# Performance work log

Hardware: AMD Instinct MI355X
Metric: run time of the kernel (lower is better)

## Reference

```python
import jax, jax.numpy as jnp
import numpy as np

VOL = (256, 256, 256)
K = 64  # number of connected components (clusters)


def setup_inputs() -> dict:
    key = jax.random.key(0)
    k1, k2, k3 = jax.random.split(key, 3)
    # Precomputed connected-component labels of (pred + target) > 0.
    # 0 = background, 1..K = clusters.
    labels = jax.random.randint(k1, VOL, 0, K + 1, dtype=jnp.int32)
    fg = labels > 0
    # Binary prediction / ground-truth masks, nonzero only inside labeled regions
    # (consistent with labels being components of the overlay of pred and target).
    pred = ((jax.random.uniform(k2, VOL) < 0.6) & fg).astype(jnp.float32)
    target = ((jax.random.uniform(k3, VOL) < 0.6) & fg).astype(jnp.float32)
    return {"pred": pred, "target": target, "labels": labels, "num_clusters": K}


def reference(pred, target, labels, num_clusters):
    # Per-cluster dice via one fused segment reduction instead of a Python loop
    # over clusters. Segment 0 is background and is dropped, matching
    # range(1, num_features + 1) in the original.
    lab = labels.reshape(-1)
    p = pred.reshape(-1)
    t = target.reshape(-1)
    nseg = num_clusters + 1
    # intersection = sum(pred_cluster * gt_cluster); pred/target are binary so
    # logical_and(...).float() products reduce to pred * target per segment.
    inter = jax.ops.segment_sum(p * t, lab, num_segments=nseg)[1:]
    sum_p = jax.ops.segment_sum(p, lab, num_segments=nseg)[1:]
    sum_t = jax.ops.segment_sum(t, lab, num_segments=nseg)[1:]
    union = sum_p + sum_t
    dice = jnp.where(union > 0, 2.0 * inter / jnp.maximum(union, 1.0), 1.0)
    return 1.0 - jnp.mean(dice)
```

## Files before the change

### kernel.cpp

```cpp
#include <hip/hip_runtime.h>


#define NSEG 65
#define NWAVES 4
#define BLOCKS 2048
#define THREADS 256

__device__ __forceinline__ unsigned long long pack_contrib(float p, float t) {
    unsigned long long sp = (p != 0.0f) ? 1ull : 0ull;
    unsigned long long st = (t != 0.0f) ? 1ull : 0ull;
    return ((sp & st) << 42) | (sp << 21) | st;
}

__device__ __forceinline__ void accum4(unsigned long long (*s_cnt)[NSEG], int wave,
                                       float4 p, float4 t, int4 l) {
    atomicAdd(&s_cnt[wave][l.x], pack_contrib(p.x, t.x));
    atomicAdd(&s_cnt[wave][l.y], pack_contrib(p.y, t.y));
    atomicAdd(&s_cnt[wave][l.z], pack_contrib(p.z, t.z));
    atomicAdd(&s_cnt[wave][l.w], pack_contrib(p.w, t.w));
}

__global__ __launch_bounds__(THREADS) void seg_count_kernel(
    const float* __restrict__ pred,
    const float* __restrict__ target,
    const int* __restrict__ labels,
    unsigned long long* __restrict__ g_counts,
    int n)
{
    __shared__ unsigned long long s_cnt[NWAVES][NSEG];
    const int tid = threadIdx.x;
    const int wave = tid >> 6;

    for (int i = tid; i < NWAVES * NSEG; i += THREADS)
        ((unsigned long long*)s_cnt)[i] = 0ull;
    __syncthreads();

    const int n_vec = n >> 2;
    const float4* __restrict__ p4 = (const float4*)pred;
    const float4* __restrict__ t4 = (const float4*)target;
    const int4*   __restrict__ l4 = (const int4*)labels;

    const int chunk = (n_vec + (int)gridDim.x - 1) / (int)gridDim.x;
    const int base = blockIdx.x * chunk;
    const int end = min(base + chunk, n_vec);

    int idx = base + tid;
    for (; idx + 3 * THREADS < end; idx += 4 * THREADS) {
        float4 p0 = p4[idx];
        float4 p1 = p4[idx + THREADS];
        float4 p2 = p4[idx + 2 * THREADS];
        float4 p3 = p4[idx + 3 * THREADS];
        float4 t0 = t4[idx];
        float4 t1 = t4[idx + THREADS];
        float4 t2 = t4[idx + 2 * THREADS];
        float4 t3 = t4[idx + 3 * THREADS];
        int4   l0 = l4[idx];
        int4   l1 = l4[idx + THREADS];
        int4   l2 = l4[idx + 2 * THREADS];
        int4   l3 = l4[idx + 3 * THREADS];
        accum4(s_cnt, wave, p0, t0, l0);
        accum4(s_cnt, wave, p1, t1, l1);
        accum4(s_cnt, wave, p2, t2, l2);
        accum4(s_cnt, wave, p3, t3, l3);
    }
    for (; idx < end; idx += THREADS)
        accum4(s_cnt, wave, p4[idx], t4[idx], l4[idx]);

    if (blockIdx.x == 0) {
        for (int i = (n_vec << 2) + tid; i < n; i += THREADS)
            atomicAdd(&s_cnt[wave][labels[i]], pack_contrib(pred[i], target[i]));
    }
    __syncthreads();

    for (int s = tid; s < NSEG; s += THREADS) {
        unsigned long long tot = 0;
        #pragma unroll
        for (int w = 0; w < NWAVES; ++w) tot += s_cnt[w][s];
        if (tot) atomicAdd(&g_counts[s], tot);
    }
}

__global__ __launch_bounds__(64) void dice_finalize_kernel(
    const unsigned long long* __restrict__ g_counts,
    const int* __restrict__ nc_ptr,
    float* __restrict__ out)
{
    const int nc = *nc_ptr;
    const int tid = threadIdx.x;
    float local = 0.0f;
    for (int c = 1 + tid; c <= nc; c += 64) {
        unsigned long long v = g_counts[c];
        float in = (float)(v >> 42);
        float sp = (float)((v >> 21) & 0x1FFFFFull);
        float st = (float)(v & 0x1FFFFFull);
        float uni = sp + st;
        local += (uni > 0.0f) ? (2.0f * in / uni) : 1.0f;
    }
    #pragma unroll
    for (int off = 32; off > 0; off >>= 1)
        local += __shfl_down(local, off);
    if (tid == 0) out[0] = 1.0f - local / (float)nc;
}

extern "C" void kernel_launch(void* const* d_in, const int* in_sizes, int n_in,
                              void* d_out, int out_size, void* d_ws, size_t ws_size,
                              hipStream_t stream) {
    const float* pred   = (const float*)d_in[0];
    const float* target = (const float*)d_in[1];
    const int*   labels = (const int*)d_in[2];
    const int*   nc_ptr = (const int*)d_in[3];
    float* out = (float*)d_out;
    unsigned long long* g_counts = (unsigned long long*)d_ws;

    const int n = in_sizes[0];

    hipMemsetAsync(d_ws, 0, NSEG * sizeof(unsigned long long), stream);

    seg_count_kernel<<<BLOCKS, THREADS, 0, stream>>>(
        pred, target, labels, g_counts, n);
    dice_finalize_kernel<<<1, 64, 0, stream>>>(g_counts, nc_ptr, out);
}
```

Baseline: 207.0 us.

## Use 32-bit packed LDS histograms with sixteen privatized copies per block

```diff
diff --git a/kernel.cpp b/kernel.cpp
--- a/kernel.cpp
+++ b/kernel.cpp
@@ -3,36 +3,39 @@
 
 #define NSEG 65
 #define NWAVES 4
+#define NSUB 4
+#define NCOPY (NWAVES * NSUB)
 #define BLOCKS 2048
 #define THREADS 256
+#define UNROLL 8
 
-__device__ __forceinline__ unsigned long long pack_contrib(float p, float t) {
-    unsigned long long sp = (p != 0.0f) ? 1ull : 0ull;
-    unsigned long long st = (t != 0.0f) ? 1ull : 0ull;
-    return ((sp & st) << 42) | (sp << 21) | st;
+__device__ __forceinline__ unsigned int pack32(float p, float t) {
+    unsigned int sp = (p != 0.0f) ? 1u : 0u;
+    unsigned int st = (t != 0.0f) ? 1u : 0u;
+    return ((sp & st) << 20) | (sp << 10) | st;
 }
 
-__device__ __forceinline__ void accum4(unsigned long long (*s_cnt)[NSEG], int wave,
+__device__ __forceinline__ void accum4(unsigned int (*s_cnt)[NSEG], int copy,
                                        float4 p, float4 t, int4 l) {
-    atomicAdd(&s_cnt[wave][l.x], pack_contrib(p.x, t.x));
-    atomicAdd(&s_cnt[wave][l.y], pack_contrib(p.y, t.y));
-    atomicAdd(&s_cnt[wave][l.z], pack_contrib(p.z, t.z));
-    atomicAdd(&s_cnt[wave][l.w], pack_contrib(p.w, t.w));
+    atomicAdd(&s_cnt[copy][l.x], pack32(p.x, t.x));
+    atomicAdd(&s_cnt[copy][l.y], pack32(p.y, t.y));
+    atomicAdd(&s_cnt[copy][l.z], pack32(p.z, t.z));
+    atomicAdd(&s_cnt[copy][l.w], pack32(p.w, t.w));
 }
 
-__global__ __launch_bounds__(THREADS) void seg_count_kernel(
+__global__ __launch_bounds__(THREADS, 4) void seg_count_kernel(
     const float* __restrict__ pred,
     const float* __restrict__ target,
     const int* __restrict__ labels,
     unsigned long long* __restrict__ g_counts,
     int n)
 {
-    __shared__ unsigned long long s_cnt[NWAVES][NSEG];
+    __shared__ unsigned int s_cnt[NCOPY][NSEG];
     const int tid = threadIdx.x;
-    const int wave = tid >> 6;
+    const int copy = tid >> 4;
 
-    for (int i = tid; i < NWAVES * NSEG; i += THREADS)
-        ((unsigned long long*)s_cnt)[i] = 0ull;
+    for (int i = tid; i < NCOPY * NSEG; i += THREADS)
+        ((unsigned int*)s_cnt)[i] = 0u;
     __syncthreads();
 
     const int n_vec = n >> 2;
@@ -45,37 +48,36 @@
     const int end = min(base + chunk, n_vec);
 
     int idx = base + tid;
-    for (; idx + 3 * THREADS < end; idx += 4 * THREADS) {
-        float4 p0 = p4[idx];
-        float4 p1 = p4[idx + THREADS];
-        float4 p2 = p4[idx + 2 * THREADS];
-        float4 p3 = p4[idx + 3 * THREADS];
-        float4 t0 = t4[idx];
-        float4 t1 = t4[idx + THREADS];
-        float4 t2 = t4[idx + 2 * THREADS];
-        float4 t3 = t4[idx + 3 * THREADS];
-        int4   l0 = l4[idx];
-        int4   l1 = l4[idx + THREADS];
-        int4   l2 = l4[idx + 2 * THREADS];
-        int4   l3 = l4[idx + 3 * THREADS];
-        accum4(s_cnt, wave, p0, t0, l0);
-        accum4(s_cnt, wave, p1, t1, l1);
-        accum4(s_cnt, wave, p2, t2, l2);
-        accum4(s_cnt, wave, p3, t3, l3);
+    for (; idx + (UNROLL - 1) * THREADS < end; idx += UNROLL * THREADS) {
+        float4 p[UNROLL]; float4 t[UNROLL]; int4 l[UNROLL];
+        #pragma unroll
+        for (int u = 0; u < UNROLL; ++u) p[u] = p4[idx + u * THREADS];
+        #pragma unroll
+        for (int u = 0; u < UNROLL; ++u) t[u] = t4[idx + u * THREADS];
+        #pragma unroll
+        for (int u = 0; u < UNROLL; ++u) l[u] = l4[idx + u * THREADS];
+        #pragma unroll
+        for (int u = 0; u < UNROLL; ++u) accum4(s_cnt, copy, p[u], t[u], l[u]);
     }
     for (; idx < end; idx += THREADS)
-        accum4(s_cnt, wave, p4[idx], t4[idx], l4[idx]);
+        accum4(s_cnt, copy, p4[idx], t4[idx], l4[idx]);
 
     if (blockIdx.x == 0) {
         for (int i = (n_vec << 2) + tid; i < n; i += THREADS)
-            atomicAdd(&s_cnt[wave][labels[i]], pack_contrib(pred[i], target[i]));
+            atomicAdd(&s_cnt[copy][labels[i]], pack32(pred[i], target[i]));
     }
     __syncthreads();
 
     for (int s = tid; s < NSEG; s += THREADS) {
-        unsigned long long tot = 0;
+        unsigned long long in = 0, sp = 0, st = 0;
         #pragma unroll
-        for (int w = 0; w < NWAVES; ++w) tot += s_cnt[w][s];
+        for (int c = 0; c < NCOPY; ++c) {
+            unsigned int v = s_cnt[c][s];
+            st += v & 0x3FFu;
+            sp += (v >> 10) & 0x3FFu;
+            in += v >> 20;
+        }
+        unsigned long long tot = (in << 42) | (sp << 21) | st;
         if (tot) atomicAdd(&g_counts[s], tot);
     }
 }
```

After: 206.3 us. About the same (-0.3%).
